# Performance work log

Measured on AMD Instinct MI355X. Metric: run time of the kernel, lower is better.

The kernel has to match this reference:

```python
import jax, jax.numpy as jnp
import numpy as np

NUM_SAMPLED = 512       # num_sampled_points
EXTRA_WIDTH = 1.0       # pool_extra_width


def setup_inputs() -> dict:
    key = jax.random.key(0)
    k1, k2, k3, k4, k5, k6 = jax.random.split(key, 6)
    B, N, C, M = 4, 16384, 128, 128
    # lidar-like points: xy in [0,40] m, z in [-2,2] m
    xy = jax.random.uniform(k1, (B, N, 2), jnp.float32, 0.0, 40.0)
    z = jax.random.uniform(k2, (B, N, 1), jnp.float32, -2.0, 2.0)
    points = jnp.concatenate([xy, z], axis=-1)
    point_features = jax.random.normal(k3, (B, N, C), jnp.float32)
    # boxes: centers in same range, dims 1-5 m, heading in [-pi, pi]
    cxy = jax.random.uniform(k4, (B, M, 2), jnp.float32, 0.0, 40.0)
    cz = jax.random.uniform(k5, (B, M, 1), jnp.float32, -1.0, 1.0)
    dims = jax.random.uniform(k6, (B, M, 3), jnp.float32, 1.0, 5.0)
    heading = jax.random.uniform(jax.random.fold_in(key, 7), (B, M, 1), jnp.float32, -3.14159, 3.14159)
    boxes3d = jnp.concatenate([cxy, cz, dims, heading], axis=-1)
    return {"points": points, "point_features": point_features, "boxes3d": boxes3d}


def _pool_one(points, feats, boxes):
    # points (N,3), feats (N,C), boxes (M,7)
    N = points.shape[0]
    center = boxes[:, 0:3]                      # (M,3)
    dims = boxes[:, 3:6] + 2.0 * EXTRA_WIDTH    # enlarge_box3d: dx,dy,dz += 2*extra
    heading = boxes[:, 6]                       # (M,)
    # shift into box-centered frame: (M,N)
    sx = points[None, :, 0] - center[:, 0:1]
    sy = points[None, :, 1] - center[:, 1:2]
    sz = points[None, :, 2] - center[:, 2:3]
    ch = jnp.cos(heading)[:, None]
    sh = jnp.sin(heading)[:, None]
    # rotate by -heading into box local frame
    lx = sx * ch + sy * sh
    ly = -sx * sh + sy * ch
    mask = (jnp.abs(lx) < dims[:, 0:1] * 0.5) \
         & (jnp.abs(ly) < dims[:, 1:2] * 0.5) \
         & (jnp.abs(sz) < dims[:, 2:3] * 0.5)   # (M,N)
    cnt = mask.sum(axis=1)                       # (M,) points in each box
    # stable order of matched point indices: matched first, in original order
    order_key = jnp.where(mask, jnp.arange(N, dtype=jnp.int32)[None, :], N)
    idx_sorted = jnp.argsort(order_key, axis=1)[:, :NUM_SAMPLED]  # (M,S)
    # slot k takes the (k mod cnt)-th matched point (wrap-around duplication)
    k = jnp.arange(NUM_SAMPLED, dtype=jnp.int32)[None, :]
    cnt_safe = jnp.maximum(cnt, 1)[:, None]
    wrapped = k % cnt_safe                       # (M,S), k when cnt>k
    gather_idx = jnp.take_along_axis(idx_sorted, wrapped, axis=1)  # (M,S)
    data = jnp.concatenate([points, feats], axis=1)  # (N,3+C)
    pooled = data[gather_idx]                    # (M,S,3+C)
    empty = (cnt == 0).astype(jnp.int32)         # (M,)
    pooled = jnp.where(empty[:, None, None] > 0, jnp.zeros((), pooled.dtype), pooled)
    return pooled, empty


def reference(points, point_features, boxes3d):
    pooled_features, pooled_empty_flag = jax.vmap(_pool_one)(points, point_features, boxes3d)
    return pooled_features, pooled_empty_flag
```

## Files before the change

### kernel.cpp

```cpp
#include <hip/hip_runtime.h>

#define BATCH 4
#define NPTS 16384
#define NBOX 128
#define NFEAT 128
#define NS 512
#define ROW 131
#define NWORDS (NPTS / 64)

__global__ __launch_bounds__(256) void roipool3d_kernel(
    const float* __restrict__ points,
    const float* __restrict__ feats,
    const float* __restrict__ boxes,
    float* __restrict__ out_pooled,
    float* __restrict__ out_flag)
{
#pragma clang fp contract(off)
    const int box_id = blockIdx.x;
    const int b      = box_id >> 7;
    const int tid    = threadIdx.x;
    const int wave   = tid >> 6;
    const int lane   = tid & 63;

    __shared__ unsigned long long s_bits[NWORDS];
    __shared__ int s_idx[NS];
    __shared__ int s_gi[NS];
    __shared__ int s_wsum[4];

    const float* bx = boxes + box_id * 7;
    const float cx = bx[0], cy = bx[1], cz = bx[2];
    const float hx = bx[3] * 0.5f + 1.0f;
    const float hy = bx[4] * 0.5f + 1.0f;
    const float hz = bx[5] * 0.5f + 1.0f;
    const double hd = (double)bx[6];
    const float ch = (float)cos(hd);
    const float sh = (float)sin(hd);

    const float* pts = points + (size_t)b * NPTS * 3;
    const float* fb  = feats  + (size_t)b * NPTS * NFEAT;

    for (int it = 0; it < NPTS / 256; ++it) {
        const int i = it * 256 + wave * 64 + lane;
        const float px = pts[i * 3 + 0];
        const float py = pts[i * 3 + 1];
        const float pz = pts[i * 3 + 2];
        const float sx = px - cx;
        const float sy = py - cy;
        const float sz = pz - cz;
        const float t0 = sx * ch;
        const float t1 = sy * sh;
        const float lx = t0 + t1;
        const float t2 = (-sx) * sh;
        const float t3 = sy * ch;
        const float ly = t2 + t3;
        const bool inside = (fabsf(lx) < hx) && (fabsf(ly) < hy) && (fabsf(sz) < hz);
        const unsigned long long m = __ballot(inside);
        if (lane == 0) s_bits[it * 4 + wave] = m;
    }
    __syncthreads();

    const unsigned long long w = s_bits[tid];
    const int pc = __popcll(w);
    int pre = pc;
    #pragma unroll
    for (int off = 1; off < 64; off <<= 1) {
        const int v = __shfl_up(pre, off);
        if (lane >= off) pre += v;
    }
    if (lane == 63) s_wsum[wave] = pre;
    __syncthreads();
    int wbase = 0;
    for (int i = 0; i < wave; ++i) wbase += s_wsum[i];
    const int total = s_wsum[0] + s_wsum[1] + s_wsum[2] + s_wsum[3];
    int pos = wbase + (pre - pc);
    unsigned long long mm = w;
    while (mm && pos < NS) {
        const int bit = __builtin_ctzll(mm);
        s_idx[pos] = tid * 64 + bit;
        ++pos;
        mm &= (mm - 1);
    }
    const int cnt = (total < NS) ? total : NS;
    __syncthreads();

    float* outp = out_pooled + (size_t)box_id * NS * ROW;

    if (cnt == 0) {
        for (int idx = tid; idx < NS * ROW; idx += 256) outp[idx] = 0.0f;
        if (tid == 0) out_flag[box_id] = 1.0f;
        return;
    }

    for (int k = tid; k < NS; k += 256) {
        const int j = (k < cnt) ? k : (k % cnt);
        s_gi[k] = s_idx[j];
    }
    __syncthreads();

    for (int idx = tid; idx < NS * ROW; idx += 256) {
        const int k  = idx / ROW;
        const int c  = idx - k * ROW;
        const int gi = s_gi[k];
        const float v = (c < 3) ? pts[gi * 3 + c] : fb[gi * NFEAT + (c - 3)];
        outp[idx] = v;
    }
    if (tid == 0) out_flag[box_id] = 0.0f;
}

extern "C" void kernel_launch(void* const* d_in, const int* in_sizes, int n_in,
                              void* d_out, int out_size, void* d_ws, size_t ws_size,
                              hipStream_t stream) {
    const float* points = (const float*)d_in[0];
    const float* feats  = (const float*)d_in[1];
    const float* boxes  = (const float*)d_in[2];
    float* out_pooled = (float*)d_out;
    float* out_flag   = out_pooled + (size_t)BATCH * NBOX * NS * ROW;

    roipool3d_kernel<<<BATCH * NBOX, 256, 0, stream>>>(
        points, feats, boxes, out_pooled, out_flag);
}
```

Before: 231.7 us.

## Split mask and gather into separate kernels with vectorized LDS-staged row copies

Splits the work into two kernels. A mask kernel computes box membership and writes compact 16-bit gather indices and counts to workspace. A gather kernel runs 16x more blocks, each covering 32 sample rows. It loads features as float4, stages the rows in LDS and writes them out as contiguous float4 stores. This is meant to remove the per-element div/mod indexing and scalar stores of the single-block-per-box gather and to raise parallelism for the memory-bound copy. In exchange it adds a second launch and a workspace round trip.

```diff
diff --git a/kernel.cpp b/kernel.cpp
--- a/kernel.cpp
+++ b/kernel.cpp
@@ -7,12 +7,14 @@
 #define NS 512
 #define ROW 131
 #define NWORDS (NPTS / 64)
+#define ROWS_PER_BLK 32
+#define SUBS (NS / ROWS_PER_BLK)
 
-__global__ __launch_bounds__(256) void roipool3d_kernel(
+__global__ __launch_bounds__(256) void mask_kernel(
     const float* __restrict__ points,
-    const float* __restrict__ feats,
     const float* __restrict__ boxes,
-    float* __restrict__ out_pooled,
+    unsigned short* __restrict__ gi_ws,
+    int* __restrict__ cnt_ws,
     float* __restrict__ out_flag)
 {
 #pragma clang fp contract(off)
@@ -24,7 +26,6 @@
 
     __shared__ unsigned long long s_bits[NWORDS];
     __shared__ int s_idx[NS];
-    __shared__ int s_gi[NS];
     __shared__ int s_wsum[4];
 
     const float* bx = boxes + box_id * 7;
@@ -37,7 +38,6 @@
     const float sh = (float)sin(hd);
 
     const float* pts = points + (size_t)b * NPTS * 3;
-    const float* fb  = feats  + (size_t)b * NPTS * NFEAT;
 
     for (int it = 0; it < NPTS / 256; ++it) {
         const int i = it * 256 + wave * 64 + lane;
@@ -83,28 +83,71 @@
     const int cnt = (total < NS) ? total : NS;
     __syncthreads();
 
-    float* outp = out_pooled + (size_t)box_id * NS * ROW;
+    if (tid == 0) {
+        cnt_ws[box_id] = cnt;
+        out_flag[box_id] = (cnt == 0) ? 1.0f : 0.0f;
+    }
+    if (cnt > 0) {
+        for (int k = tid; k < NS; k += 256) {
+            const int j = (k < cnt) ? k : (k % cnt);
+            gi_ws[box_id * NS + k] = (unsigned short)s_idx[j];
+        }
+    }
+}
+
+__global__ __launch_bounds__(256) void gather_kernel(
+    const float* __restrict__ points,
+    const float* __restrict__ feats,
+    const unsigned short* __restrict__ gi_ws,
+    const int* __restrict__ cnt_ws,
+    float* __restrict__ out_pooled)
+{
+    const int blk    = blockIdx.x;
+    const int box_id = blk >> 4;
+    const int sub    = blk & (SUBS - 1);
+    const int b      = box_id >> 7;
+    const int tid    = threadIdx.x;
+    const int wave   = tid >> 6;
+    const int lane   = tid & 63;
+
+    __shared__ float s_row[ROWS_PER_BLK * ROW];
+    __shared__ unsigned short s_gi[ROWS_PER_BLK];
+
+    const int cnt = cnt_ws[box_id];
+    float* outg = out_pooled + (size_t)blk * (ROWS_PER_BLK * ROW);
 
     if (cnt == 0) {
-        for (int idx = tid; idx < NS * ROW; idx += 256) outp[idx] = 0.0f;
-        if (tid == 0) out_flag[box_id] = 1.0f;
+        float4 z = make_float4(0.f, 0.f, 0.f, 0.f);
+        float4* og = (float4*)outg;
+        for (int i = tid; i < (ROWS_PER_BLK * ROW) / 4; i += 256) og[i] = z;
         return;
     }
 
-    for (int k = tid; k < NS; k += 256) {
-        const int j = (k < cnt) ? k : (k % cnt);
-        s_gi[k] = s_idx[j];
+    if (tid < ROWS_PER_BLK) s_gi[tid] = gi_ws[box_id * NS + sub * ROWS_PER_BLK + tid];
+    __syncthreads();
+
+    const float* pts = points + (size_t)b * NPTS * 3;
+    const float* fb  = feats  + (size_t)b * NPTS * NFEAT;
+
+    const int cg = lane & 31;
+    const int rh = lane >> 5;
+    #pragma unroll
+    for (int it = 0; it < 4; ++it) {
+        const int row = wave * 8 + it * 2 + rh;
+        const int gi  = s_gi[row];
+        const float4 f = *(const float4*)(fb + (size_t)gi * NFEAT + cg * 4);
+        float* sr = s_row + row * ROW;
+        sr[3 + cg * 4 + 0] = f.x;
+        sr[3 + cg * 4 + 1] = f.y;
+        sr[3 + cg * 4 + 2] = f.z;
+        sr[3 + cg * 4 + 3] = f.w;
+        if (cg < 3) sr[cg] = pts[gi * 3 + cg];
     }
     __syncthreads();
 
-    for (int idx = tid; idx < NS * ROW; idx += 256) {
-        const int k  = idx / ROW;
-        const int c  = idx - k * ROW;
-        const int gi = s_gi[k];
-        const float v = (c < 3) ? pts[gi * 3 + c] : fb[gi * NFEAT + (c - 3)];
-        outp[idx] = v;
-    }
-    if (tid == 0) out_flag[box_id] = 0.0f;
+    const float4* sv = (const float4*)s_row;
+    float4* og = (float4*)outg;
+    for (int i = tid; i < (ROWS_PER_BLK * ROW) / 4; i += 256) og[i] = sv[i];
 }
 
 extern "C" void kernel_launch(void* const* d_in, const int* in_sizes, int n_in,
@@ -116,6 +159,9 @@
     float* out_pooled = (float*)d_out;
     float* out_flag   = out_pooled + (size_t)BATCH * NBOX * NS * ROW;
 
-    roipool3d_kernel<<<BATCH * NBOX, 256, 0, stream>>>(
-        points, feats, boxes, out_pooled, out_flag);
+    unsigned short* gi_ws = (unsigned short*)d_ws;
+    int* cnt_ws = (int*)(gi_ws + (size_t)BATCH * NBOX * NS);
+
+    mask_kernel<<<BATCH * NBOX, 256, 0, stream>>>(points, boxes, gi_ws, cnt_ws, out_flag);
+    gather_kernel<<<BATCH * NBOX * SUBS, 256, 0, stream>>>(points, feats, gi_ws, cnt_ws, out_pooled);
 }
```

Result: faster. 212.1 us (-8.5%).
